# Kernel tuning notes

Hardware: AMD Instinct MI355X
Metric: run time of the kernel (lower is better)

## Reference

```python
import jax, jax.numpy as jnp
import numpy as np

B, Ca, Cv, NH = 4, 128, 512, 8
Ta, F, Tv = 64, 64, 256
EPS = 1e-5


def group_norm(x, gamma, beta):
    # num_groups=1 GroupNorm: normalize over all non-batch axes, per-channel affine.
    axes = tuple(range(1, x.ndim))
    mu = jnp.mean(x, axis=axes, keepdims=True)
    var = jnp.mean((x - mu) ** 2, axis=axes, keepdims=True)
    xn = (x - mu) * jax.lax.rsqrt(var + EPS)
    shape = (1, -1) + (1,) * (x.ndim - 2)
    return xn * gamma.reshape(shape) + beta.reshape(shape)


def setup_inputs() -> dict:
    key = jax.random.key(0)
    ks = jax.random.split(key, 10)
    s = 0.1
    inp = {
        'audio': jax.random.normal(ks[0], (B, Ca, Ta, F), jnp.float32),
        'video': jax.random.normal(ks[1], (B, Cv, Tv), jnp.float32),
        # grouped 1x1 convs have weight shape (Cout,1,1[,1]) -> flatten to (Cout,)
        'p1_w': jax.random.normal(ks[2], (Cv,), jnp.float32) * s,
        'p1_b': jnp.zeros((Cv,), jnp.float32),
        'p1_g': jnp.ones((Cv,), jnp.float32),
        'p1_be': jnp.zeros((Cv,), jnp.float32),
        'p2_w': jax.random.normal(ks[3], (Cv,), jnp.float32) * s,
        'p2_b': jnp.zeros((Cv,), jnp.float32),
        'p2_g': jnp.ones((Cv,), jnp.float32),
        'p2_be': jnp.zeros((Cv,), jnp.float32),
        'f1_w': jax.random.normal(ks[4], (Cv * NH,), jnp.float32) * s,
        'f1_b': jnp.zeros((Cv * NH,), jnp.float32),
        'f1_g': jnp.ones((Cv * NH,), jnp.float32),
        'f1_be': jnp.zeros((Cv * NH,), jnp.float32),
        'f2_w': jax.random.normal(ks[5], (Cv,), jnp.float32) * s,
        'f2_b': jnp.zeros((Cv,), jnp.float32),
        'f2_g': jnp.ones((Cv,), jnp.float32),
        'f2_be': jnp.zeros((Cv,), jnp.float32),
    }
    return inp


def reference(audio, video, p1_w, p1_b, p1_g, p1_be, p2_w, p2_b, p2_g, p2_be,
              f1_w, f1_b, f1_g, f1_be, f2_w, f2_b, f2_g, f2_be):
    Bx, Cax, Tax, Fx = audio.shape
    _, Cvx, Tvx = video.shape
    rep = Cvx // Cax
    Hx = f1_w.shape[0] // Cvx

    # grouped 1x1 Conv2d (groups=Ca): out channel c reads input channel c // rep
    a_exp = jnp.repeat(audio, rep, axis=1)                      # (B, Cv, Ta, F)
    a_val = group_norm(a_exp * p1_w[None, :, None, None] + p1_b[None, :, None, None], p1_g, p1_be)
    a_gate = jax.nn.relu(group_norm(a_exp * p2_w[None, :, None, None] + p2_b[None, :, None, None], p2_g, p2_be))

    # nearest interpolation Ta -> Tv (F unchanged): src = floor(dst * Ta / Tv)
    idx = (jnp.arange(Tvx) * Tax) // Tvx
    a_val = a_val[:, :, idx, :]                                  # (B, Cv, Tv, F)
    a_gate = a_gate[:, :, idx, :]

    # grouped 1x1 Conv1d f1 (groups=Cv, out=Cv*H): out channel g*H+h reads channel g
    v_rep = jnp.repeat(video, Hx, axis=1)                        # (B, Cv*H, Tv)
    vh = group_norm(v_rep * f1_w[None, :, None] + f1_b[None, :, None], f1_g, f1_be)
    vh = vh.reshape(Bx, Cvx, Hx, Tvx)
    vm = jnp.mean(vh, axis=2)                                    # (B, Cv, Tv)
    v_attn = jax.nn.softmax(vm, axis=-1)

    # grouped 1x1 Conv1d f2 (groups=Cv): per-channel scale
    v_key = group_norm(video * f2_w[None, :, None] + f2_b[None, :, None], f2_g, f2_be)

    fusion = jnp.sum(a_val * v_attn[..., None] + a_gate * v_key[..., None], axis=-1)  # (B, Cv, Tv)
    return fusion + video
```

## Files before the change

kernel.cpp:

```cpp
#include <hip/hip_runtime.h>

#define NB 4
#define CA 128
#define CV 512
#define NHH 8
#define TA 64
#define FF 64
#define TV 256
#define REPC 4
#define EPSV 1e-5f


__device__ __forceinline__ float waveReduceSum(float x) {
  #pragma unroll
  for (int off = 32; off; off >>= 1) x += __shfl_xor(x, off);
  return x;
}
__device__ __forceinline__ float waveReduceMax(float x) {
  #pragma unroll
  for (int off = 32; off; off >>= 1) x = fmaxf(x, __shfl_xor(x, off));
  return x;
}
__device__ __forceinline__ float group16ReduceSum(float x) {
  #pragma unroll
  for (int off = 8; off; off >>= 1) x += __shfl_xor(x, off);
  return x;
}

__global__ __launch_bounds__(256) void stats_kernel(
    const float* __restrict__ audio, const float* __restrict__ video,
    const float* __restrict__ p1_w, const float* __restrict__ p1_b,
    const float* __restrict__ p2_w, const float* __restrict__ p2_b,
    const float* __restrict__ f1_w, const float* __restrict__ f1_b,
    const float* __restrict__ f2_w, const float* __restrict__ f2_b,
    float* __restrict__ ws)
{
  const int bid = blockIdx.x;
  const int tid = threadIdx.x;
  const int wv = tid >> 6, ln = tid & 63;
  __shared__ float red1[4], red2[4], fold[4][4];

  if (bid < NB * CA) {
    const int b = bid >> 7, ca = bid & (CA - 1);
    const float4* ap4 = (const float4*)(audio + (size_t)(b * CA + ca) * (TA * FF));
    float s = 0.f, q = 0.f;
    #pragma unroll
    for (int i = 0; i < 4; ++i) {
      float4 v = ap4[tid + i * 256];
      s += v.x + v.y + v.z + v.w;
      q += v.x * v.x + v.y * v.y + v.z * v.z + v.w * v.w;
    }
    s = waveReduceSum(s); q = waveReduceSum(q);
    if (ln == 0) { red1[wv] = s; red2[wv] = q; }
    __syncthreads();
    if (tid == 0) {
      float S = red1[0] + red1[1] + red1[2] + red1[3];
      float Q = red2[0] + red2[1] + red2[2] + red2[3];
      float W1 = 0, W1q = 0, W1pb = 0, C1 = 0, C1q = 0;
      float W2 = 0, W2q = 0, W2pb = 0, C2 = 0, C2q = 0;
      #pragma unroll
      for (int r = 0; r < REPC; ++r) {
        int c = ca * REPC + r;
        float w = p1_w[c], bb = p1_b[c];
        W1 += w; W1q += w * w; W1pb += w * bb; C1 += bb; C1q += bb * bb;
        float w2 = p2_w[c], b2 = p2_b[c];
        W2 += w2; W2q += w2 * w2; W2pb += w2 * b2; C2 += b2; C2q += b2 * b2;
      }
      const float NE = (float)(TA * FF);
      const int base = b * 128 + ca;
      ws[0 * 512 + base] = W1 * S + NE * C1;
      ws[1 * 512 + base] = W1q * Q + 2.f * W1pb * S + NE * C1q;
      ws[2 * 512 + base] = W2 * S + NE * C2;
      ws[3 * 512 + base] = W2q * Q + 2.f * W2pb * S + NE * C2q;
    }
  } else {
    const int vb = bid - NB * CA;
    const int b = vb >> 7, vi = vb & 127;
    const int c = vi * 4 + wv;
    const float4* vp4 = (const float4*)(video + (size_t)(b * CV + c) * TV);
    float4 v = vp4[ln];
    float s = v.x + v.y + v.z + v.w;
    float q = v.x * v.x + v.y * v.y + v.z * v.z + v.w * v.w;
    s = waveReduceSum(s); q = waveReduceSum(q);
    if (ln == 0) {
      float Wf = 0, Wfq = 0, Wfb = 0, Cf = 0, Cfq = 0;
      #pragma unroll
      for (int h = 0; h < NHH; ++h) {
        int j = c * NHH + h;
        float fw = f1_w[j], fb = f1_b[j];
        Wf += fw; Wfq += fw * fw; Wfb += fw * fb; Cf += fb; Cfq += fb * fb;
      }
      const float NT = (float)TV;
      float w2 = f2_w[c], b2 = f2_b[c];
      fold[wv][0] = Wf * s + NT * Cf;
      fold[wv][1] = Wfq * q + 2.f * Wfb * s + NT * Cfq;
      fold[wv][2] = w2 * s + NT * b2;
      fold[wv][3] = w2 * w2 * q + 2.f * w2 * b2 * s + NT * b2 * b2;
    }
    __syncthreads();
    if (tid < 4) {
      float p = fold[0][tid] + fold[1][tid] + fold[2][tid] + fold[3][tid];
      ws[(4 + tid) * 512 + b * 128 + vi] = p;
    }
  }
}

__global__ __launch_bounds__(256) void out_kernel(
    const float* __restrict__ audio, const float* __restrict__ video,
    const float* __restrict__ p1_w, const float* __restrict__ p1_b,
    const float* __restrict__ p1_g, const float* __restrict__ p1_be,
    const float* __restrict__ p2_w, const float* __restrict__ p2_b,
    const float* __restrict__ p2_g, const float* __restrict__ p2_be,
    const float* __restrict__ f1_w, const float* __restrict__ f1_g,
    const float* __restrict__ f2_w, const float* __restrict__ f2_b,
    const float* __restrict__ f2_g, const float* __restrict__ f2_be,
    const float* __restrict__ ws, float* __restrict__ out)
{
  const int bid = blockIdx.x;
  const int b = bid >> 7;
  const int ca = bid & (CA - 1);
  const int c0 = ca * 4;
  const int tid = threadIdx.x;
  const int wv = tid >> 6, ln = tid & 63;

  __shared__ float acc8[8];
  __shared__ float ssa[TA];
  __shared__ float sg[4][TA];

  #pragma unroll
  for (int r = 0; r < 2; ++r) {
    int qq = wv * 2 + r;
    const float* p = ws + qq * 512 + b * 128;
    float s = p[ln] + p[64 + ln];
    s = waveReduceSum(s);
    if (ln == 0) acc8[qq] = s;
  }
  __syncthreads();

  const float invNa = 1.f / (float)(CV * TA * FF);
  const float invN3 = 1.f / (float)(CV * NHH * TV);
  const float invN4 = 1.f / (float)(CV * TV);
  float mu1 = acc8[0] * invNa;
  float rs1 = rsqrtf(fmaxf(acc8[1] * invNa - mu1 * mu1, 0.f) + EPSV);
  float mu2 = acc8[2] * invNa;
  float rs2 = rsqrtf(fmaxf(acc8[3] * invNa - mu2 * mu2, 0.f) + EPSV);
  float mu3 = acc8[4] * invN3;
  float rs3 = rsqrtf(fmaxf(acc8[5] * invN3 - mu3 * mu3, 0.f) + EPSV);
  float mu4 = acc8[6] * invN4;
  float rs4 = rsqrtf(fmaxf(acc8[7] * invN4 - mu4 * mu4, 0.f) + EPSV);

  float A2a[4], B2a[4];
  #pragma unroll
  for (int cc = 0; cc < 4; ++cc) {
    int c = c0 + cc;
    A2a[cc] = p2_w[c] * rs2 * p2_g[c];
    B2a[cc] = (p2_b[c] - mu2) * rs2 * p2_g[c] + p2_be[c];
  }

  const float4* ap4 = (const float4*)(audio + (size_t)(b * CA + ca) * (TA * FF));
  #pragma unroll
  for (int i = 0; i < 4; ++i) {
    int rbase = wv * 16 + i * 4;
    float4 v = ap4[rbase * 16 + ln];
    float sa = v.x + v.y + v.z + v.w;
    float g0 = fmaxf(v.x * A2a[0] + B2a[0], 0.f) + fmaxf(v.y * A2a[0] + B2a[0], 0.f)
             + fmaxf(v.z * A2a[0] + B2a[0], 0.f) + fmaxf(v.w * A2a[0] + B2a[0], 0.f);
    float g1 = fmaxf(v.x * A2a[1] + B2a[1], 0.f) + fmaxf(v.y * A2a[1] + B2a[1], 0.f)
             + fmaxf(v.z * A2a[1] + B2a[1], 0.f) + fmaxf(v.w * A2a[1] + B2a[1], 0.f);
    float g2 = fmaxf(v.x * A2a[2] + B2a[2], 0.f) + fmaxf(v.y * A2a[2] + B2a[2], 0.f)
             + fmaxf(v.z * A2a[2] + B2a[2], 0.f) + fmaxf(v.w * A2a[2] + B2a[2], 0.f);
    float g3 = fmaxf(v.x * A2a[3] + B2a[3], 0.f) + fmaxf(v.y * A2a[3] + B2a[3], 0.f)
             + fmaxf(v.z * A2a[3] + B2a[3], 0.f) + fmaxf(v.w * A2a[3] + B2a[3], 0.f);
    sa = group16ReduceSum(sa);
    g0 = group16ReduceSum(g0);
    g1 = group16ReduceSum(g1);
    g2 = group16ReduceSum(g2);
    g3 = group16ReduceSum(g3);
    if ((ln & 15) == 0) {
      int rr = rbase + (ln >> 4);
      ssa[rr] = sa;
      sg[0][rr] = g0; sg[1][rr] = g1; sg[2][rr] = g2; sg[3][rr] = g3;
    }
  }

  const int c = c0 + wv;
  const float A1 = p1_w[c] * rs1 * p1_g[c];
  const float B1 = (p1_b[c] - mu1) * rs1 * p1_g[c] + p1_be[c];
  float sw = 0.f;
  #pragma unroll
  for (int h = 0; h < NHH; ++h) sw += f1_w[c * NHH + h] * f1_g[c * NHH + h];
  const float alpha = rs3 * sw * (1.f / NHH);
  const float A4 = f2_w[c] * rs4 * f2_g[c];
  const float B4 = (f2_b[c] - mu4) * rs4 * f2_g[c] + f2_be[c];

  __syncthreads();

  const float4* vp4 = (const float4*)(video + (size_t)(b * CV + c) * TV);
  float4 v = vp4[ln];
  float l0 = alpha * v.x, l1 = alpha * v.y, l2 = alpha * v.z, l3 = alpha * v.w;
  float m = waveReduceMax(fmaxf(fmaxf(l0, l1), fmaxf(l2, l3)));
  float e0 = __expf(l0 - m), e1 = __expf(l1 - m), e2 = __expf(l2 - m), e3 = __expf(l3 - m);
  float z = waveReduceSum(e0 + e1 + e2 + e3);
  float iz = 1.f / z;
  float sval = A1 * ssa[ln] + (float)FF * B1;
  float sgate = sg[wv][ln];
  float4 o;
  o.x = e0 * iz * sval + (v.x * A4 + B4) * sgate + v.x;
  o.y = e1 * iz * sval + (v.y * A4 + B4) * sgate + v.y;
  o.z = e2 * iz * sval + (v.z * A4 + B4) * sgate + v.z;
  o.w = e3 * iz * sval + (v.w * A4 + B4) * sgate + v.w;
  ((float4*)(out + (size_t)(b * CV + c) * TV))[ln] = o;
}

extern "C" void kernel_launch(void* const* d_in, const int* in_sizes, int n_in,
                              void* d_out, int out_size, void* d_ws, size_t ws_size,
                              hipStream_t stream) {
  const float* audio = (const float*)d_in[0];
  const float* video = (const float*)d_in[1];
  const float* p1_w  = (const float*)d_in[2];
  const float* p1_b  = (const float*)d_in[3];
  const float* p1_g  = (const float*)d_in[4];
  const float* p1_be = (const float*)d_in[5];
  const float* p2_w  = (const float*)d_in[6];
  const float* p2_b  = (const float*)d_in[7];
  const float* p2_g  = (const float*)d_in[8];
  const float* p2_be = (const float*)d_in[9];
  const float* f1_w  = (const float*)d_in[10];
  const float* f1_b  = (const float*)d_in[11];
  const float* f1_g  = (const float*)d_in[12];
  const float* f2_w  = (const float*)d_in[14];
  const float* f2_b  = (const float*)d_in[15];
  const float* f2_g  = (const float*)d_in[16];
  const float* f2_be = (const float*)d_in[17];
  (void)in_sizes; (void)n_in; (void)out_size; (void)ws_size;

  float* ws  = (float*)d_ws;
  float* out = (float*)d_out;

  stats_kernel<<<NB * CA + NB * CV / 4, 256, 0, stream>>>(
      audio, video, p1_w, p1_b, p2_w, p2_b, f1_w, f1_b, f2_w, f2_b, ws);

  out_kernel<<<NB * CA, 256, 0, stream>>>(
      audio, video,
      p1_w, p1_b, p1_g, p1_be,
      p2_w, p2_b, p2_g, p2_be,
      f1_w, f1_g, f2_w, f2_b, f2_g, f2_be,
      ws, out);
}
```

Baseline: 15.30 us.

## Merge audio and video stats blocks and hoist loads ahead of reductions

The stats kernel now has each block handle both one audio channel group and the four matching video channels, which halves the grid and issues all global loads up front. The output kernel issues its audio, video and parameter loads before the workspace reduction and barrier, so memory latency overlaps the stats combination. The audio row mapping changes so each lane holds four float4s of one row, replacing 16-lane shuffle reductions with 4-lane ones. The cost is higher register pressure and fewer blocks in the stats launch.

```diff
diff --git a/kernel.cpp b/kernel.cpp
--- a/kernel.cpp
+++ b/kernel.cpp
@@ -21,9 +21,9 @@
   for (int off = 32; off; off >>= 1) x = fmaxf(x, __shfl_xor(x, off));
   return x;
 }
-__device__ __forceinline__ float group16ReduceSum(float x) {
-  #pragma unroll
-  for (int off = 8; off; off >>= 1) x += __shfl_xor(x, off);
+__device__ __forceinline__ float group4ReduceSum(float x) {
+  x += __shfl_xor(x, 1);
+  x += __shfl_xor(x, 2);
   return x;
 }
 
@@ -36,72 +36,73 @@
     float* __restrict__ ws)
 {
   const int bid = blockIdx.x;
+  const int b = bid >> 7, ca = bid & (CA - 1);
+  const int c0 = ca * 4;
   const int tid = threadIdx.x;
   const int wv = tid >> 6, ln = tid & 63;
+  const int c = c0 + wv;
   __shared__ float red1[4], red2[4], fold[4][4];
 
-  if (bid < NB * CA) {
-    const int b = bid >> 7, ca = bid & (CA - 1);
-    const float4* ap4 = (const float4*)(audio + (size_t)(b * CA + ca) * (TA * FF));
-    float s = 0.f, q = 0.f;
+  const float4* ap4 = (const float4*)(audio + (size_t)(b * CA + ca) * (TA * FF));
+  float4 a0 = ap4[tid];
+  float4 a1 = ap4[tid + 256];
+  float4 a2 = ap4[tid + 512];
+  float4 a3 = ap4[tid + 768];
+  const float4* vp4 = (const float4*)(video + (size_t)(b * CV + c) * TV);
+  float4 v = vp4[ln];
+
+  float s = a0.x + a0.y + a0.z + a0.w + a1.x + a1.y + a1.z + a1.w
+          + a2.x + a2.y + a2.z + a2.w + a3.x + a3.y + a3.z + a3.w;
+  float q = a0.x * a0.x + a0.y * a0.y + a0.z * a0.z + a0.w * a0.w
+          + a1.x * a1.x + a1.y * a1.y + a1.z * a1.z + a1.w * a1.w
+          + a2.x * a2.x + a2.y * a2.y + a2.z * a2.z + a2.w * a2.w
+          + a3.x * a3.x + a3.y * a3.y + a3.z * a3.z + a3.w * a3.w;
+  s = waveReduceSum(s); q = waveReduceSum(q);
+  if (ln == 0) { red1[wv] = s; red2[wv] = q; }
+
+  float vs = v.x + v.y + v.z + v.w;
+  float vq = v.x * v.x + v.y * v.y + v.z * v.z + v.w * v.w;
+  vs = waveReduceSum(vs); vq = waveReduceSum(vq);
+  if (ln == 0) {
+    float Wf = 0, Wfq = 0, Wfb = 0, Cf = 0, Cfq = 0;
     #pragma unroll
-    for (int i = 0; i < 4; ++i) {
-      float4 v = ap4[tid + i * 256];
-      s += v.x + v.y + v.z + v.w;
-      q += v.x * v.x + v.y * v.y + v.z * v.z + v.w * v.w;
+    for (int h = 0; h < NHH; ++h) {
+      int j = c * NHH + h;
+      float fw = f1_w[j], fb = f1_b[j];
+      Wf += fw; Wfq += fw * fw; Wfb += fw * fb; Cf += fb; Cfq += fb * fb;
     }
-    s = waveReduceSum(s); q = waveReduceSum(q);
-    if (ln == 0) { red1[wv] = s; red2[wv] = q; }
-    __syncthreads();
-    if (tid == 0) {
-      float S = red1[0] + red1[1] + red1[2] + red1[3];
-      float Q = red2[0] + red2[1] + red2[2] + red2[3];
-      float W1 = 0, W1q = 0, W1pb = 0, C1 = 0, C1q = 0;
-      float W2 = 0, W2q = 0, W2pb = 0, C2 = 0, C2q = 0;
-      #pragma unroll
-      for (int r = 0; r < REPC; ++r) {
-        int c = ca * REPC + r;
-        float w = p1_w[c], bb = p1_b[c];
-        W1 += w; W1q += w * w; W1pb += w * bb; C1 += bb; C1q += bb * bb;
-        float w2 = p2_w[c], b2 = p2_b[c];
-        W2 += w2; W2q += w2 * w2; W2pb += w2 * b2; C2 += b2; C2q += b2 * b2;
-      }
-      const float NE = (float)(TA * FF);
-      const int base = b * 128 + ca;
-      ws[0 * 512 + base] = W1 * S + NE * C1;
-      ws[1 * 512 + base] = W1q * Q + 2.f * W1pb * S + NE * C1q;
-      ws[2 * 512 + base] = W2 * S + NE * C2;
-      ws[3 * 512 + base] = W2q * Q + 2.f * W2pb * S + NE * C2q;
+    const float NT = (float)TV;
+    float w2 = f2_w[c], b2 = f2_b[c];
+    fold[wv][0] = Wf * vs + NT * Cf;
+    fold[wv][1] = Wfq * vq + 2.f * Wfb * vs + NT * Cfq;
+    fold[wv][2] = w2 * vs + NT * b2;
+    fold[wv][3] = w2 * w2 * vq + 2.f * w2 * b2 * vs + NT * b2 * b2;
+  }
+  __syncthreads();
+  if (tid == 0) {
+    float S = red1[0] + red1[1] + red1[2] + red1[3];
+    float Q = red2[0] + red2[1] + red2[2] + red2[3];
+    float W1 = 0, W1q = 0, W1pb = 0, C1 = 0, C1q = 0;
+    float W2 = 0, W2q = 0, W2pb = 0, C2 = 0, C2q = 0;
+    #pragma unroll
+    for (int r = 0; r < REPC; ++r) {
+      int c2 = c0 + r;
+      float w = p1_w[c2], bb = p1_b[c2];
+      W1 += w; W1q += w * w; W1pb += w * bb; C1 += bb; C1q += bb * bb;
+      float w2 = p2_w[c2], b2 = p2_b[c2];
+      W2 += w2; W2q += w2 * w2; W2pb += w2 * b2; C2 += b2; C2q += b2 * b2;
     }
-  } else {
-    const int vb = bid - NB * CA;
-    const int b = vb >> 7, vi = vb & 127;
-    const int c = vi * 4 + wv;
-    const float4* vp4 = (const float4*)(video + (size_t)(b * CV + c) * TV);
-    float4 v = vp4[ln];
-    float s = v.x + v.y + v.z + v.w;
-    float q = v.x * v.x + v.y * v.y + v.z * v.z + v.w * v.w;
-    s = waveReduceSum(s); q = waveReduceSum(q);
-    if (ln == 0) {
-      float Wf = 0, Wfq = 0, Wfb = 0, Cf = 0, Cfq = 0;
-      #pragma unroll
-      for (int h = 0; h < NHH; ++h) {
-        int j = c * NHH + h;
-        float fw = f1_w[j], fb = f1_b[j];
-        Wf += fw; Wfq += fw * fw; Wfb += fw * fb; Cf += fb; Cfq += fb * fb;
-      }
-      const float NT = (float)TV;
-      float w2 = f2_w[c], b2 = f2_b[c];
-      fold[wv][0] = Wf * s + NT * Cf;
-      fold[wv][1] = Wfq * q + 2.f * Wfb * s + NT * Cfq;
-      fold[wv][2] = w2 * s + NT * b2;
-      fold[wv][3] = w2 * w2 * q + 2.f * w2 * b2 * s + NT * b2 * b2;
-    }
-    __syncthreads();
-    if (tid < 4) {
-      float p = fold[0][tid] + fold[1][tid] + fold[2][tid] + fold[3][tid];
-      ws[(4 + tid) * 512 + b * 128 + vi] = p;
-    }
+    const float NE = (float)(TA * FF);
+    const int base = b * 128 + ca;
+    ws[0 * 512 + base] = W1 * S + NE * C1;
+    ws[1 * 512 + base] = W1q * Q + 2.f * W1pb * S + NE * C1q;
+    ws[2 * 512 + base] = W2 * S + NE * C2;
+    ws[3 * 512 + base] = W2q * Q + 2.f * W2pb * S + NE * C2q;
+  }
+  if (tid >= 4 && tid < 8) {
+    int k = tid - 4;
+    float p = fold[0][k] + fold[1][k] + fold[2][k] + fold[3][k];
+    ws[(4 + k) * 512 + b * 128 + ca] = p;
   }
 }
 
@@ -122,10 +123,30 @@
   const int c0 = ca * 4;
   const int tid = threadIdx.x;
   const int wv = tid >> 6, ln = tid & 63;
+  const int c = c0 + wv;
+  const int row = wv * 16 + (ln >> 2);
+  const int lq = ln & 3;
 
   __shared__ float acc8[8];
   __shared__ float ssa[TA];
   __shared__ float sg[4][TA];
+
+  const float4* ap4 = (const float4*)(audio + (size_t)(b * CA + ca) * (TA * FF));
+  const int abase = row * 16 + lq;
+  float4 av0 = ap4[abase];
+  float4 av1 = ap4[abase + 4];
+  float4 av2 = ap4[abase + 8];
+  float4 av3 = ap4[abase + 12];
+  const float4* vp4 = (const float4*)(video + (size_t)(b * CV + c) * TV);
+  float4 v = vp4[ln];
+  float4 p2w4  = ((const float4*)p2_w)[ca];
+  float4 p2b4  = ((const float4*)p2_b)[ca];
+  float4 p2g4  = ((const float4*)p2_g)[ca];
+  float4 p2be4 = ((const float4*)p2_be)[ca];
+  float p1wv = p1_w[c], p1bv = p1_b[c], p1gv = p1_g[c], p1bev = p1_be[c];
+  float4 f1wa = ((const float4*)f1_w)[c * 2], f1wb = ((const float4*)f1_w)[c * 2 + 1];
+  float4 f1ga = ((const float4*)f1_g)[c * 2], f1gb = ((const float4*)f1_g)[c * 2 + 1];
+  float f2wv = f2_w[c], f2bv = f2_b[c], f2gv = f2_g[c], f2bev = f2_be[c];
 
   #pragma unroll
   for (int r = 0; r < 2; ++r) {
@@ -150,53 +171,46 @@
   float rs4 = rsqrtf(fmaxf(acc8[7] * invN4 - mu4 * mu4, 0.f) + EPSV);
 
   float A2a[4], B2a[4];
+  A2a[0] = p2w4.x * rs2 * p2g4.x;  B2a[0] = (p2b4.x - mu2) * rs2 * p2g4.x + p2be4.x;
+  A2a[1] = p2w4.y * rs2 * p2g4.y;  B2a[1] = (p2b4.y - mu2) * rs2 * p2g4.y + p2be4.y;
+  A2a[2] = p2w4.z * rs2 * p2g4.z;  B2a[2] = (p2b4.z - mu2) * rs2 * p2g4.z + p2be4.z;
+  A2a[3] = p2w4.w * rs2 * p2g4.w;  B2a[3] = (p2b4.w - mu2) * rs2 * p2g4.w + p2be4.w;
+
+  float sa = av0.x + av0.y + av0.z + av0.w + av1.x + av1.y + av1.z + av1.w
+           + av2.x + av2.y + av2.z + av2.w + av3.x + av3.y + av3.z + av3.w;
+  float g[4];
   #pragma unroll
   for (int cc = 0; cc < 4; ++cc) {
-    int c = c0 + cc;
-    A2a[cc] = p2_w[c] * rs2 * p2_g[c];
-    B2a[cc] = (p2_b[c] - mu2) * rs2 * p2_g[c] + p2_be[c];
-  }
-
-  const float4* ap4 = (const float4*)(audio + (size_t)(b * CA + ca) * (TA * FF));
-  #pragma unroll
-  for (int i = 0; i < 4; ++i) {
-    int rbase = wv * 16 + i * 4;
-    float4 v = ap4[rbase * 16 + ln];
-    float sa = v.x + v.y + v.z + v.w;
-    float g0 = fmaxf(v.x * A2a[0] + B2a[0], 0.f) + fmaxf(v.y * A2a[0] + B2a[0], 0.f)
-             + fmaxf(v.z * A2a[0] + B2a[0], 0.f) + fmaxf(v.w * A2a[0] + B2a[0], 0.f);
-    float g1 = fmaxf(v.x * A2a[1] + B2a[1], 0.f) + fmaxf(v.y * A2a[1] + B2a[1], 0.f)
-             + fmaxf(v.z * A2a[1] + B2a[1], 0.f) + fmaxf(v.w * A2a[1] + B2a[1], 0.f);
-    float g2 = fmaxf(v.x * A2a[2] + B2a[2], 0.f) + fmaxf(v.y * A2a[2] + B2a[2], 0.f)
-             + fmaxf(v.z * A2a[2] + B2a[2], 0.f) + fmaxf(v.w * A2a[2] + B2a[2], 0.f);
-    float g3 = fmaxf(v.x * A2a[3] + B2a[3], 0.f) + fmaxf(v.y * A2a[3] + B2a[3], 0.f)
-             + fmaxf(v.z * A2a[3] + B2a[3], 0.f) + fmaxf(v.w * A2a[3] + B2a[3], 0.f);
-    sa = group16ReduceSum(sa);
-    g0 = group16ReduceSum(g0);
-    g1 = group16ReduceSum(g1);
-    g2 = group16ReduceSum(g2);
-    g3 = group16ReduceSum(g3);
-    if ((ln & 15) == 0) {
-      int rr = rbase + (ln >> 4);
-      ssa[rr] = sa;
-      sg[0][rr] = g0; sg[1][rr] = g1; sg[2][rr] = g2; sg[3][rr] = g3;
-    }
-  }
-
-  const int c = c0 + wv;
-  const float A1 = p1_w[c] * rs1 * p1_g[c];
-  const float B1 = (p1_b[c] - mu1) * rs1 * p1_g[c] + p1_be[c];
-  float sw = 0.f;
-  #pragma unroll
-  for (int h = 0; h < NHH; ++h) sw += f1_w[c * NHH + h] * f1_g[c * NHH + h];
+    float A = A2a[cc], Bv = B2a[cc];
+    g[cc] = fmaxf(av0.x * A + Bv, 0.f) + fmaxf(av0.y * A + Bv, 0.f)
+          + fmaxf(av0.z * A + Bv, 0.f) + fmaxf(av0.w * A + Bv, 0.f)
+          + fmaxf(av1.x * A + Bv, 0.f) + fmaxf(av1.y * A + Bv, 0.f)
+          + fmaxf(av1.z * A + Bv, 0.f) + fmaxf(av1.w * A + Bv, 0.f)
+          + fmaxf(av2.x * A + Bv, 0.f) + fmaxf(av2.y * A + Bv, 0.f)
+          + fmaxf(av2.z * A + Bv, 0.f) + fmaxf(av2.w * A + Bv, 0.f)
+          + fmaxf(av3.x * A + Bv, 0.f) + fmaxf(av3.y * A + Bv, 0.f)
+          + fmaxf(av3.z * A + Bv, 0.f) + fmaxf(av3.w * A + Bv, 0.f);
+  }
+  sa = group4ReduceSum(sa);
+  g[0] = group4ReduceSum(g[0]);
+  g[1] = group4ReduceSum(g[1]);
+  g[2] = group4ReduceSum(g[2]);
+  g[3] = group4ReduceSum(g[3]);
+  if (lq == 0) {
+    ssa[row] = sa;
+    sg[0][row] = g[0]; sg[1][row] = g[1]; sg[2][row] = g[2]; sg[3][row] = g[3];
+  }
+
+  const float A1 = p1wv * rs1 * p1gv;
+  const float B1 = (p1bv - mu1) * rs1 * p1gv + p1bev;
+  float sw = f1wa.x * f1ga.x + f1wa.y * f1ga.y + f1wa.z * f1ga.z + f1wa.w * f1ga.w
+           + f1wb.x * f1gb.x + f1wb.y * f1gb.y + f1wb.z * f1gb.z + f1wb.w * f1gb.w;
   const float alpha = rs3 * sw * (1.f / NHH);
-  const float A4 = f2_w[c] * rs4 * f2_g[c];
-  const float B4 = (f2_b[c] - mu4) * rs4 * f2_g[c] + f2_be[c];
+  const float A4 = f2wv * rs4 * f2gv;
+  const float B4 = (f2bv - mu4) * rs4 * f2gv + f2bev;
 
   __syncthreads();
 
-  const float4* vp4 = (const float4*)(video + (size_t)(b * CV + c) * TV);
-  float4 v = vp4[ln];
   float l0 = alpha * v.x, l1 = alpha * v.y, l2 = alpha * v.z, l3 = alpha * v.w;
   float m = waveReduceMax(fmaxf(fmaxf(l0, l1), fmaxf(l2, l3)));
   float e0 = __expf(l0 - m), e1 = __expf(l1 - m), e2 = __expf(l2 - m), e3 = __expf(l3 - m);
@@ -237,7 +251,7 @@
   float* ws  = (float*)d_ws;
   float* out = (float*)d_out;
 
-  stats_kernel<<<NB * CA + NB * CV / 4, 256, 0, stream>>>(
+  stats_kernel<<<NB * CA, 256, 0, stream>>>(
       audio, video, p1_w, p1_b, p2_w, p2_b, f1_w, f1_b, f2_w, f2_b, ws);
 
   out_kernel<<<NB * CA, 256, 0, stream>>>(
```

Measured after the change: 14.33 us. 6.3% less time.
